# Kernel optimization log

Hardware: AMD Instinct MI355X
Metric: run time of the kernel (lower is better)

The kernel has to match this reference:

```python
import jax, jax.numpy as jnp
import numpy as np

# module hyperparameters (from init_kwargs): kernel_size=(KH,KW), stride_size=(SH,SW)
KH, KW = 8, 8
SH, SW = 4, 4


def setup_inputs() -> dict:
    key = jax.random.key(0)
    x = jax.random.normal(key, (8, 64, 96, 96), dtype=jnp.float32)
    return {"x": x}


def _local_autocorr(x):
    """Local window self-correlation.

    For each kH x kW window (extracted with stride (SH,SW)), compute the
    correlation of the window with itself shifted by every offset
    (dy - KH//2, dx - KW//2), dy in [0,KH), dx in [0,KW), zero-padded
    outside the window. Output: [B, C, nH, nW, KH, KW].
    """
    B, C, H, W = x.shape
    nH = (H - KH) // SH + 1
    nW = (W - KW) // SW + 1
    # window gather indices
    ys = (jnp.arange(nH) * SH)[:, None] + jnp.arange(KH)[None, :]  # [nH, KH]
    xs = (jnp.arange(nW) * SW)[:, None] + jnp.arange(KW)[None, :]  # [nW, KW]
    # [B, C, nH, KH, nW, KW] -> [N, KH, KW], N = B*C*nH*nW
    patches = x[:, :, ys[:, :, None, None], xs[None, None, :, :]]
    patches = patches.transpose(0, 1, 2, 4, 3, 5).reshape(-1, KH, KW)
    N = patches.shape[0]
    # zero-pad each window so every shift stays in-bounds
    pt, pb = KH // 2, KH - 1 - KH // 2
    pl, pr = KW // 2, KW - 1 - KW // 2
    padded = jnp.pad(patches, ((0, 0), (pt, pb), (pl, pr)))  # [N, 2KH-1, 2KW-1]
    # depthwise (per-window) cross-correlation: out[n, dy, dx] =
    #   sum_{y,x} padded[n, dy + y, dx + x] * patches[n, y, x]
    out = jax.lax.conv_general_dilated(
        padded[None],           # [1, N, 2KH-1, 2KW-1]
        patches[:, None],       # [N, 1, KH, KW]
        window_strides=(1, 1),
        padding='VALID',
        dimension_numbers=('NCHW', 'OIHW', 'NCHW'),
        feature_group_count=N,
    )[0]                        # [N, KH, KW]
    return out.reshape(B, C, nH, nW, KH, KW)


def reference(x):
    return _local_autocorr(x)
```

## Files before the change

kernel.cpp:

```cpp
#include <hip/hip_runtime.h>


constexpr int KH = 8, KW = 8, SH = 4, SW = 4;
constexpr int B = 8, C = 64, H = 96, W = 96;
constexpr int nH = (H - KH) / SH + 1;
constexpr int nW = (W - KW) / SW + 1;
constexpr int NWIN = B * C * nH * nW;
constexpr int TPB = 256;
constexpr int WPB = 64;
constexpr int OSTRIDE = 65;
constexpr int NBLK = NWIN / WPB;
constexpr int NXCD = 8;
constexpr int CPX = NBLK / NXCD;

__global__ __launch_bounds__(TPB, 4) void
local_autocorr_kernel(const float* __restrict__ x, float* __restrict__ out) {
    __shared__ float lds[WPB * OSTRIDE];

    const int tid  = threadIdx.x;
    const int role = tid >> 6;
    const int k    = tid & 63;

    const int bid = (int)blockIdx.x;
    const int blk = (bid % NXCD) * CPX + bid / NXCD;
    const int n = blk * WPB + k;

    const int w  = n % nW;
    const int tt = n / nW;
    const int h  = tt % nH;
    const int bc = tt / nH;

    const float* xp = x + ((size_t)bc * H + (size_t)h * SH) * W + (size_t)w * SW;

    float* slot = &lds[k * OSTRIDE];

#define LOADROW(dst, ri)                                                              \
    {                                                                                 \
        const float4 lo_ = *reinterpret_cast<const float4*>(xp + (size_t)(ri)*W);     \
        const float4 hi_ = *reinterpret_cast<const float4*>(xp + (size_t)(ri)*W + 4); \
        dst[0]=lo_.x; dst[1]=lo_.y; dst[2]=lo_.z; dst[3]=lo_.w;                       \
        dst[4]=hi_.x; dst[5]=hi_.y; dst[6]=hi_.z; dst[7]=hi_.w;                       \
    }

#define FMABLK(ACC, AROW, BROW)                                                       \
    {                                                                                 \
        _Pragma("unroll")                                                             \
        for (int dx = 0; dx < 8; ++dx) {                                              \
            const int OX = dx - 4;                                                    \
            _Pragma("unroll")                                                         \
            for (int j = 0; j < 8; ++j) {                                             \
                if (j + OX < 0 || j + OX >= 8) continue;              \
                ACC[dx] = fmaf(AROW[j + OX], BROW[j], ACC[dx]);                       \
            }                                                                         \
        }                                                                             \
    }

#define CELLF(CC, AROW, BROW)                                                         \
    {                                                                                 \
        CC = fmaf(BROW[0], AROW[4], CC); CC = fmaf(BROW[1], AROW[5], CC);             \
        CC = fmaf(BROW[2], AROW[6], CC); CC = fmaf(BROW[3], AROW[7], CC);             \
    }

    if (role == 0) {
        float a0[8], a4[8];
#pragma unroll
        for (int dx = 0; dx < 8; ++dx) { a0[dx] = 0.f; a4[dx] = 0.f; }
        float cur[8], aux[8];
#pragma unroll
        for (int r = 0; r < 8; ++r) {
            LOADROW(cur, r)
            FMABLK(a0, cur, cur)
            if (r >= 4) {
                LOADROW(aux, r - 4)
                FMABLK(a4, aux, cur)
            }
            __builtin_amdgcn_sched_barrier(0);
        }
        *reinterpret_cast<float4*>(slot + 0)  = make_float4(a4[0], a4[1], a4[2], a4[3]);
        *reinterpret_cast<float4*>(slot + 4)  = make_float4(a4[4], a4[5], a4[6], a4[7]);
        *reinterpret_cast<float4*>(slot + 32) = make_float4(a0[0], a0[1], a0[2], a0[3]);
        *reinterpret_cast<float4*>(slot + 36) = make_float4(a0[4], a0[5], a0[6], a0[7]);
    } else if (role == 1) {
        float a1[8]; float c50 = 0.f;
#pragma unroll
        for (int dx = 0; dx < 8; ++dx) a1[dx] = 0.f;
        float rr[2][8];
        LOADROW(rr[0], 0)
#pragma unroll
        for (int r = 1; r < 8; ++r) {
            LOADROW(rr[r & 1], r)
            FMABLK(a1, rr[(r - 1) & 1], rr[r & 1])
            CELLF(c50, rr[(r - 1) & 1], rr[r & 1])
            __builtin_amdgcn_sched_barrier(0);
        }
        *reinterpret_cast<float4*>(slot + 24) = make_float4(a1[0], a1[1], a1[2], a1[3]);
        *reinterpret_cast<float4*>(slot + 28) = make_float4(a1[4], a1[5], a1[6], a1[7]);
        *reinterpret_cast<float4*>(slot + 40) = make_float4(c50,   a1[7], a1[6], a1[5]);
        *reinterpret_cast<float4*>(slot + 44) = make_float4(a1[4], a1[3], a1[2], a1[1]);
    } else if (role == 2) {
        float a2[8]; float c60 = 0.f;
#pragma unroll
        for (int dx = 0; dx < 8; ++dx) a2[dx] = 0.f;
        float cur[8], aux[8];
#pragma unroll
        for (int r = 2; r < 8; ++r) {
            LOADROW(cur, r)
            LOADROW(aux, r - 2)
            FMABLK(a2, aux, cur)
            CELLF(c60, aux, cur)
            __builtin_amdgcn_sched_barrier(0);
        }
        *reinterpret_cast<float4*>(slot + 16) = make_float4(a2[0], a2[1], a2[2], a2[3]);
        *reinterpret_cast<float4*>(slot + 20) = make_float4(a2[4], a2[5], a2[6], a2[7]);
        *reinterpret_cast<float4*>(slot + 48) = make_float4(c60,   a2[7], a2[6], a2[5]);
        *reinterpret_cast<float4*>(slot + 52) = make_float4(a2[4], a2[3], a2[2], a2[1]);
    } else {
        float a3[8]; float c70 = 0.f;
#pragma unroll
        for (int dx = 0; dx < 8; ++dx) a3[dx] = 0.f;
        float cur[8], aux[8];
#pragma unroll
        for (int r = 3; r < 8; ++r) {
            LOADROW(cur, r)
            LOADROW(aux, r - 3)
            FMABLK(a3, aux, cur)
            CELLF(c70, aux, cur)
            __builtin_amdgcn_sched_barrier(0);
        }
        *reinterpret_cast<float4*>(slot + 8)  = make_float4(a3[0], a3[1], a3[2], a3[3]);
        *reinterpret_cast<float4*>(slot + 12) = make_float4(a3[4], a3[5], a3[6], a3[7]);
        *reinterpret_cast<float4*>(slot + 56) = make_float4(c70,   a3[7], a3[6], a3[5]);
        *reinterpret_cast<float4*>(slot + 60) = make_float4(a3[4], a3[3], a3[2], a3[1]);
    }
#undef LOADROW
#undef FMABLK
#undef CELLF

    __syncthreads();

    float* obase = out + (size_t)blk * WPB * 64;
#pragma unroll
    for (int kk = 0; kk < 4; ++kk) {
        const int flat4 = tid + kk * TPB;
        const float4 v = *reinterpret_cast<const float4*>(
            &lds[(flat4 >> 4) * OSTRIDE + (flat4 & 15) * 4]);
        *reinterpret_cast<float4*>(obase + (size_t)flat4 * 4) = v;
    }
}

extern "C" void kernel_launch(void* const* d_in, const int* in_sizes, int n_in,
                              void* d_out, int out_size, void* d_ws, size_t ws_size,
                              hipStream_t stream) {
    const float* x = (const float*)d_in[0];
    float* out = (float*)d_out;

    local_autocorr_kernel<<<NBLK, TPB, 0, stream>>>(x, out);
}
```

Measured before the change: 32.41 us.

## Process two windows per thread with rebalanced two-role split and remainder-aware XCD swizzle

Halves the block to 128 threads while doubling windows per block to 128. Each thread now computes two windows. The work is split into two roles: role 0 does row offsets 0 and 1, role 1 does offsets 2–4, with row loads reused across offsets and the per-row sched barriers removed. Results go out in two LDS staging phases with extra barriers, and the XCD block swizzle now handles a block count that is not divisible by 8. The aim is more ILP and fewer redundant row loads per window, at the cost of higher register pressure, lower occupancy (launch bounds 2) and an extra synchronisation round.

```diff
diff --git a/kernel.cpp b/kernel.cpp
--- a/kernel.cpp
+++ b/kernel.cpp
@@ -6,38 +6,43 @@
 constexpr int nH = (H - KH) / SH + 1;
 constexpr int nW = (W - KW) / SW + 1;
 constexpr int NWIN = B * C * nH * nW;
-constexpr int TPB = 256;
-constexpr int WPB = 64;
+constexpr int TPB = 128;
+constexpr int WPB = 128;
 constexpr int OSTRIDE = 65;
 constexpr int NBLK = NWIN / WPB;
 constexpr int NXCD = 8;
-constexpr int CPX = NBLK / NXCD;
+constexpr int SWZ_Q = NBLK / NXCD;
+constexpr int SWZ_R = NBLK % NXCD;
 
-__global__ __launch_bounds__(TPB, 4) void
+__global__ __launch_bounds__(TPB, 2) void
 local_autocorr_kernel(const float* __restrict__ x, float* __restrict__ out) {
-    __shared__ float lds[WPB * OSTRIDE];
+    __shared__ float lds[64 * OSTRIDE];
 
     const int tid  = threadIdx.x;
     const int role = tid >> 6;
     const int k    = tid & 63;
 
     const int bid = (int)blockIdx.x;
-    const int blk = (bid % NXCD) * CPX + bid / NXCD;
-    const int n = blk * WPB + k;
+    const int xcd = bid & 7;
+    const int idx = bid >> 3;
+    const int blk = (xcd < SWZ_R ? xcd * (SWZ_Q + 1)
+                                 : SWZ_R * (SWZ_Q + 1) + (xcd - SWZ_R) * SWZ_Q) + idx;
 
-    const int w  = n % nW;
-    const int tt = n / nW;
-    const int h  = tt % nH;
-    const int bc = tt / nH;
+    const int n0 = blk * WPB + k;
+    const int n1 = n0 + 64;
 
-    const float* xp = x + ((size_t)bc * H + (size_t)h * SH) * W + (size_t)w * SW;
+    const int w0  = n0 % nW;  const int t0 = n0 / nW;
+    const int h0  = t0 % nH;  const int bc0 = t0 / nH;
+    const int w1  = n1 % nW;  const int t1 = n1 / nW;
+    const int h1  = t1 % nH;  const int bc1 = t1 / nH;
 
-    float* slot = &lds[k * OSTRIDE];
+    const float* xp0 = x + ((size_t)bc0 * H + (size_t)h0 * SH) * W + (size_t)w0 * SW;
+    const float* xp1 = x + ((size_t)bc1 * H + (size_t)h1 * SH) * W + (size_t)w1 * SW;
 
-#define LOADROW(dst, ri)                                                              \
+#define LOADROW(dst, xp, ri)                                                          \
     {                                                                                 \
-        const float4 lo_ = *reinterpret_cast<const float4*>(xp + (size_t)(ri)*W);     \
-        const float4 hi_ = *reinterpret_cast<const float4*>(xp + (size_t)(ri)*W + 4); \
+        const float4 lo_ = *reinterpret_cast<const float4*>((xp) + (size_t)(ri)*W);   \
+        const float4 hi_ = *reinterpret_cast<const float4*>((xp) + (size_t)(ri)*W+4); \
         dst[0]=lo_.x; dst[1]=lo_.y; dst[2]=lo_.z; dst[3]=lo_.w;                       \
         dst[4]=hi_.x; dst[5]=hi_.y; dst[6]=hi_.z; dst[7]=hi_.w;                       \
     }
@@ -61,90 +66,105 @@
         CC = fmaf(BROW[2], AROW[6], CC); CC = fmaf(BROW[3], AROW[7], CC);             \
     }
 
+    float a0w0[8], a1w0[8], a0w1[8], a1w1[8];
+    float a2w0[8], a3w0[8], a4w0[8], a2w1[8], a3w1[8], a4w1[8];
+    float c50w0 = 0.f, c50w1 = 0.f;
+    float c60w0 = 0.f, c70w0 = 0.f, c60w1 = 0.f, c70w1 = 0.f;
+
     if (role == 0) {
-        float a0[8], a4[8];
 #pragma unroll
-        for (int dx = 0; dx < 8; ++dx) { a0[dx] = 0.f; a4[dx] = 0.f; }
-        float cur[8], aux[8];
-#pragma unroll
-        for (int r = 0; r < 8; ++r) {
-            LOADROW(cur, r)
-            FMABLK(a0, cur, cur)
-            if (r >= 4) {
-                LOADROW(aux, r - 4)
-                FMABLK(a4, aux, cur)
-            }
-            __builtin_amdgcn_sched_barrier(0);
+        for (int dx = 0; dx < 8; ++dx) {
+            a0w0[dx] = 0.f; a1w0[dx] = 0.f; a0w1[dx] = 0.f; a1w1[dx] = 0.f;
         }
-        *reinterpret_cast<float4*>(slot + 0)  = make_float4(a4[0], a4[1], a4[2], a4[3]);
-        *reinterpret_cast<float4*>(slot + 4)  = make_float4(a4[4], a4[5], a4[6], a4[7]);
-        *reinterpret_cast<float4*>(slot + 32) = make_float4(a0[0], a0[1], a0[2], a0[3]);
-        *reinterpret_cast<float4*>(slot + 36) = make_float4(a0[4], a0[5], a0[6], a0[7]);
-    } else if (role == 1) {
-        float a1[8]; float c50 = 0.f;
-#pragma unroll
-        for (int dx = 0; dx < 8; ++dx) a1[dx] = 0.f;
-        float rr[2][8];
-        LOADROW(rr[0], 0)
+        float r0_[3][8], r1_[3][8];
+        LOADROW(r0_[0], xp0, 0) LOADROW(r1_[0], xp1, 0)
+        LOADROW(r0_[1], xp0, 1) LOADROW(r1_[1], xp1, 1)
+        FMABLK(a0w0, r0_[0], r0_[0])
+        FMABLK(a0w1, r1_[0], r1_[0])
 #pragma unroll
         for (int r = 1; r < 8; ++r) {
-            LOADROW(rr[r & 1], r)
-            FMABLK(a1, rr[(r - 1) & 1], rr[r & 1])
-            CELLF(c50, rr[(r - 1) & 1], rr[r & 1])
-            __builtin_amdgcn_sched_barrier(0);
+            if (r < 7) { LOADROW(r0_[(r + 1) % 3], xp0, r + 1)
+                         LOADROW(r1_[(r + 1) % 3], xp1, r + 1) }
+            FMABLK(a0w0, r0_[r % 3], r0_[r % 3])
+            FMABLK(a0w1, r1_[r % 3], r1_[r % 3])
+            FMABLK(a1w0, r0_[(r - 1) % 3], r0_[r % 3])
+            CELLF(c50w0, r0_[(r - 1) % 3], r0_[r % 3])
+            FMABLK(a1w1, r1_[(r - 1) % 3], r1_[r % 3])
+            CELLF(c50w1, r1_[(r - 1) % 3], r1_[r % 3])
         }
-        *reinterpret_cast<float4*>(slot + 24) = make_float4(a1[0], a1[1], a1[2], a1[3]);
-        *reinterpret_cast<float4*>(slot + 28) = make_float4(a1[4], a1[5], a1[6], a1[7]);
-        *reinterpret_cast<float4*>(slot + 40) = make_float4(c50,   a1[7], a1[6], a1[5]);
-        *reinterpret_cast<float4*>(slot + 44) = make_float4(a1[4], a1[3], a1[2], a1[1]);
-    } else if (role == 2) {
-        float a2[8]; float c60 = 0.f;
+    } else {
 #pragma unroll
-        for (int dx = 0; dx < 8; ++dx) a2[dx] = 0.f;
-        float cur[8], aux[8];
+        for (int dx = 0; dx < 8; ++dx) {
+            a2w0[dx] = 0.f; a3w0[dx] = 0.f; a4w0[dx] = 0.f;
+            a2w1[dx] = 0.f; a3w1[dx] = 0.f; a4w1[dx] = 0.f;
+        }
+        float cc0[2][8], cc1[2][8], aux0[8], aux1[8];
+        LOADROW(cc0[0], xp0, 2) LOADROW(cc1[0], xp1, 2)
 #pragma unroll
         for (int r = 2; r < 8; ++r) {
-            LOADROW(cur, r)
-            LOADROW(aux, r - 2)
-            FMABLK(a2, aux, cur)
-            CELLF(c60, aux, cur)
-            __builtin_amdgcn_sched_barrier(0);
+            if (r < 7) { LOADROW(cc0[(r + 1) & 1], xp0, r + 1)
+                         LOADROW(cc1[(r + 1) & 1], xp1, r + 1) }
+            LOADROW(aux0, xp0, r - 2) LOADROW(aux1, xp1, r - 2)
+            FMABLK(a2w0, aux0, cc0[r & 1]) CELLF(c60w0, aux0, cc0[r & 1])
+            FMABLK(a2w1, aux1, cc1[r & 1]) CELLF(c60w1, aux1, cc1[r & 1])
+            if (r >= 3) {
+                LOADROW(aux0, xp0, r - 3) LOADROW(aux1, xp1, r - 3)
+                FMABLK(a3w0, aux0, cc0[r & 1]) CELLF(c70w0, aux0, cc0[r & 1])
+                FMABLK(a3w1, aux1, cc1[r & 1]) CELLF(c70w1, aux1, cc1[r & 1])
+            }
+            if (r >= 4) {
+                LOADROW(aux0, xp0, r - 4) LOADROW(aux1, xp1, r - 4)
+                FMABLK(a4w0, aux0, cc0[r & 1])
+                FMABLK(a4w1, aux1, cc1[r & 1])
+            }
         }
-        *reinterpret_cast<float4*>(slot + 16) = make_float4(a2[0], a2[1], a2[2], a2[3]);
-        *reinterpret_cast<float4*>(slot + 20) = make_float4(a2[4], a2[5], a2[6], a2[7]);
-        *reinterpret_cast<float4*>(slot + 48) = make_float4(c60,   a2[7], a2[6], a2[5]);
-        *reinterpret_cast<float4*>(slot + 52) = make_float4(a2[4], a2[3], a2[2], a2[1]);
-    } else {
-        float a3[8]; float c70 = 0.f;
-#pragma unroll
-        for (int dx = 0; dx < 8; ++dx) a3[dx] = 0.f;
-        float cur[8], aux[8];
-#pragma unroll
-        for (int r = 3; r < 8; ++r) {
-            LOADROW(cur, r)
-            LOADROW(aux, r - 3)
-            FMABLK(a3, aux, cur)
-            CELLF(c70, aux, cur)
-            __builtin_amdgcn_sched_barrier(0);
-        }
-        *reinterpret_cast<float4*>(slot + 8)  = make_float4(a3[0], a3[1], a3[2], a3[3]);
-        *reinterpret_cast<float4*>(slot + 12) = make_float4(a3[4], a3[5], a3[6], a3[7]);
-        *reinterpret_cast<float4*>(slot + 56) = make_float4(c70,   a3[7], a3[6], a3[5]);
-        *reinterpret_cast<float4*>(slot + 60) = make_float4(a3[4], a3[3], a3[2], a3[1]);
     }
 #undef LOADROW
 #undef FMABLK
 #undef CELLF
 
-    __syncthreads();
-
     float* obase = out + (size_t)blk * WPB * 64;
 #pragma unroll
-    for (int kk = 0; kk < 4; ++kk) {
-        const int flat4 = tid + kk * TPB;
-        const float4 v = *reinterpret_cast<const float4*>(
-            &lds[(flat4 >> 4) * OSTRIDE + (flat4 & 15) * 4]);
-        *reinterpret_cast<float4*>(obase + (size_t)flat4 * 4) = v;
+    for (int ph = 0; ph < 2; ++ph) {
+        {
+            float* slot = &lds[k * OSTRIDE];
+            if (role == 0) {
+                const float* A0 = ph ? a0w1 : a0w0;
+                const float* A1 = ph ? a1w1 : a1w0;
+                const float  C5 = ph ? c50w1 : c50w0;
+                *reinterpret_cast<float4*>(slot + 24) = make_float4(A1[0], A1[1], A1[2], A1[3]);
+                *reinterpret_cast<float4*>(slot + 28) = make_float4(A1[4], A1[5], A1[6], A1[7]);
+                *reinterpret_cast<float4*>(slot + 32) = make_float4(A0[0], A0[1], A0[2], A0[3]);
+                *reinterpret_cast<float4*>(slot + 36) = make_float4(A0[4], A0[5], A0[6], A0[7]);
+                *reinterpret_cast<float4*>(slot + 40) = make_float4(C5,    A1[7], A1[6], A1[5]);
+                *reinterpret_cast<float4*>(slot + 44) = make_float4(A1[4], A1[3], A1[2], A1[1]);
+            } else {
+                const float* A2 = ph ? a2w1 : a2w0;
+                const float* A3 = ph ? a3w1 : a3w0;
+                const float* A4 = ph ? a4w1 : a4w0;
+                const float  C6 = ph ? c60w1 : c60w0;
+                const float  C7 = ph ? c70w1 : c70w0;
+                *reinterpret_cast<float4*>(slot + 0)  = make_float4(A4[0], A4[1], A4[2], A4[3]);
+                *reinterpret_cast<float4*>(slot + 4)  = make_float4(A4[4], A4[5], A4[6], A4[7]);
+                *reinterpret_cast<float4*>(slot + 8)  = make_float4(A3[0], A3[1], A3[2], A3[3]);
+                *reinterpret_cast<float4*>(slot + 12) = make_float4(A3[4], A3[5], A3[6], A3[7]);
+                *reinterpret_cast<float4*>(slot + 16) = make_float4(A2[0], A2[1], A2[2], A2[3]);
+                *reinterpret_cast<float4*>(slot + 20) = make_float4(A2[4], A2[5], A2[6], A2[7]);
+                *reinterpret_cast<float4*>(slot + 48) = make_float4(C6,    A2[7], A2[6], A2[5]);
+                *reinterpret_cast<float4*>(slot + 52) = make_float4(A2[4], A2[3], A2[2], A2[1]);
+                *reinterpret_cast<float4*>(slot + 56) = make_float4(C7,    A3[7], A3[6], A3[5]);
+                *reinterpret_cast<float4*>(slot + 60) = make_float4(A3[4], A3[3], A3[2], A3[1]);
+            }
+        }
+        __syncthreads();
+#pragma unroll
+        for (int kk = 0; kk < 8; ++kk) {
+            const int flat4 = tid + kk * TPB;
+            const float4 v = *reinterpret_cast<const float4*>(
+                &lds[(flat4 >> 4) * OSTRIDE + (flat4 & 15) * 4]);
+            *reinterpret_cast<float4*>(obase + (size_t)ph * 64 * 64 + flat4 * 4) = v;
+        }
+        __syncthreads();
     }
 }
 
```

After: 55.25 us. +70.5%, slower.
